# Performance work log

Measured on AMD Instinct MI355X. Metric: run time of the kernel, lower is better.

Reference implementation:

```python
import math
import jax, jax.numpy as jnp
import numpy as np

DILATION = 1  # init_kwargs

def _sep2(x, krow, kcol, d):
    # 2-tap separable correlation with circular 'same' padding:
    # pad-right + conv2d(kernel=[k0,k1]) == k0*x + k1*roll(x, -d, axis)
    xh = kcol[0] * x + kcol[1] * jnp.roll(x, -d, axis=-1)   # along W
    xv = krow[0] * xh + krow[1] * jnp.roll(xh, -d, axis=-2)  # along H
    return xv

def setup_inputs() -> dict:
    key = jax.random.key(0)
    ks = jax.random.split(key, 4)
    B, C, H, W = 8, 64, 256, 256
    LL = jax.random.normal(ks[0], (B, C, H, W), dtype=jnp.float32)
    LH = jax.random.normal(ks[1], (B, C, H, W), dtype=jnp.float32)
    HL = jax.random.normal(ks[2], (B, C, H, W), dtype=jnp.float32)
    HH = jax.random.normal(ks[3], (B, C, H, W), dtype=jnp.float32)
    s = math.sqrt(2.0)
    # torch: lor = [1/s,1/s].flip(0) = [1/s,1/s]; hir = [-1/s,1/s].flip(0) = [1/s,-1/s]
    lor = jnp.array([1.0 / s, 1.0 / s], dtype=jnp.float32)
    hir = jnp.array([1.0 / s, -1.0 / s], dtype=jnp.float32)
    return {"LL": LL, "LH": LH, "HL": HL, "HH": HH, "lor": lor, "hir": hir}

def reference(LL, LH, HL, HH, lor, hir):
    d = DILATION
    rec = (_sep2(LL, lor, lor, d)
           + _sep2(LH, lor, hir, d)
           + _sep2(HL, hir, lor, d)
           + _sep2(HH, hir, hir, d))
    rec = jnp.roll(rec, shift=(1, 1), axis=(-2, -1))
    return 0.25 * rec
```

## Files before the change

kernel.cpp:

```cpp
#include <hip/hip_runtime.h>


static constexpr int HH_ = 256;
static constexpr int WW_ = 256;
static constexpr int RPT = 16;

typedef float f4 __attribute__((ext_vector_type(4)));

__global__ __launch_bounds__(256) void swt_inv_kernel(
    const float* __restrict__ LL, const float* __restrict__ LH,
    const float* __restrict__ HL, const float* __restrict__ HH,
    float* __restrict__ out)
{
    const int slab  = blockIdx.x & 3;
    const int plane = blockIdx.x >> 2;
    const size_t poff = (size_t)plane * (HH_ * WW_);

    const int tx = threadIdx.x & 63;
    const int ty = threadIdx.x >> 6;
    const int w  = tx << 2;
    const int h0 = slab * 64 + ty * RPT;
    const int srcLane = (tx + 63) & 63;

    const float* ll = LL + poff + w;
    const float* lh = LH + poff + w;
    const float* hl = HL + poff + w;
    const float* hh = HH + poff + w;
    float* op = out + poff + w;

    const int hp = (h0 == 0) ? (HH_ - 1) : (h0 - 1);
    f4 Pp, Rp;
    {
        const int r = hp * WW_;
        f4 a = *(const f4*)(ll + r);
        f4 b = *(const f4*)(lh + r);
        f4 c = *(const f4*)(hl + r);
        f4 d = *(const f4*)(hh + r);
        f4 u0 = a + b, u1 = a - b, v0 = c + d, v1 = c - d;
        Pp = u0 + v0;
        Rp = u1 + v1;
    }

    #pragma unroll 4
    for (int i = 0; i < RPT; ++i) {
        const int r = (h0 + i) * WW_;
        f4 a = *(const f4*)(ll + r);
        f4 b = *(const f4*)(lh + r);
        f4 c = *(const f4*)(hl + r);
        f4 d = *(const f4*)(hh + r);

        f4 u0 = a + b, u1 = a - b, v0 = c + d, v1 = c - d;
        f4 Aq = Pp + (u0 - v0);
        f4 Bq = Rp + (u1 - v1);
        Pp = u0 + v0;
        Rp = u1 + v1;

        const float Am = __shfl(Aq.w, srcLane, 64);

        f4 o;
        o.x = 0.125f * (Am   + Bq.x);
        o.y = 0.125f * (Aq.x + Bq.y);
        o.z = 0.125f * (Aq.y + Bq.z);
        o.w = 0.125f * (Aq.z + Bq.w);
        __builtin_nontemporal_store(o, (f4*)(op + r));
    }
}

extern "C" void kernel_launch(void* const* d_in, const int* in_sizes, int n_in,
                              void* d_out, int out_size, void* d_ws, size_t ws_size,
                              hipStream_t stream) {
    const float* LL = (const float*)d_in[0];
    const float* LH = (const float*)d_in[1];
    const float* HL = (const float*)d_in[2];
    const float* HH = (const float*)d_in[3];
    float* out = (float*)d_out;

    const int planes = out_size / (HH_ * WW_);
    dim3 grid(planes * 4);
    dim3 block(256);
    swt_inv_kernel<<<grid, block, 0, stream>>>(LL, LH, HL, HH, out);
}
```

Before: 476.3 us.

## Halve block size, double slabs per plane, and software-prefetch next row

Blocks shrink from 256 to 128 threads, with each plane split into 8 slabs instead of 4, so the grid doubles while each thread still handles 16 rows. The row loop is fully unrolled and now loads row i+1 while computing row i, which hides global load latency behind arithmetic. The cost is more registers for the prefetched values and more redundant halo-row loads across the extra slabs.

```diff
diff --git a/kernel.cpp b/kernel.cpp
--- a/kernel.cpp
+++ b/kernel.cpp
@@ -4,22 +4,23 @@
 static constexpr int HH_ = 256;
 static constexpr int WW_ = 256;
 static constexpr int RPT = 16;
+static constexpr int SLABS = HH_ / (2 * RPT);
 
 typedef float f4 __attribute__((ext_vector_type(4)));
 
-__global__ __launch_bounds__(256) void swt_inv_kernel(
+__global__ __launch_bounds__(128) void swt_inv_kernel(
     const float* __restrict__ LL, const float* __restrict__ LH,
     const float* __restrict__ HL, const float* __restrict__ HH,
     float* __restrict__ out)
 {
-    const int slab  = blockIdx.x & 3;
-    const int plane = blockIdx.x >> 2;
+    const int slab  = blockIdx.x & (SLABS - 1);
+    const int plane = blockIdx.x >> 3;
     const size_t poff = (size_t)plane * (HH_ * WW_);
 
     const int tx = threadIdx.x & 63;
     const int ty = threadIdx.x >> 6;
     const int w  = tx << 2;
-    const int h0 = slab * 64 + ty * RPT;
+    const int h0 = slab * (2 * RPT) + ty * RPT;
     const int srcLane = (tx + 63) & 63;
 
     const float* ll = LL + poff + w;
@@ -41,15 +42,25 @@
         Rp = u1 + v1;
     }
 
-    #pragma unroll 4
+    f4 a0 = *(const f4*)(ll + h0 * WW_);
+    f4 b0 = *(const f4*)(lh + h0 * WW_);
+    f4 c0 = *(const f4*)(hl + h0 * WW_);
+    f4 d0 = *(const f4*)(hh + h0 * WW_);
+
+    #pragma unroll
     for (int i = 0; i < RPT; ++i) {
-        const int r = (h0 + i) * WW_;
-        f4 a = *(const f4*)(ll + r);
-        f4 b = *(const f4*)(lh + r);
-        f4 c = *(const f4*)(hl + r);
-        f4 d = *(const f4*)(hh + r);
+        const int rc = (h0 + i) * WW_;
 
-        f4 u0 = a + b, u1 = a - b, v0 = c + d, v1 = c - d;
+        f4 a1, b1, c1, d1;
+        if (i + 1 < RPT) {
+            const int rn = rc + WW_;
+            a1 = *(const f4*)(ll + rn);
+            b1 = *(const f4*)(lh + rn);
+            c1 = *(const f4*)(hl + rn);
+            d1 = *(const f4*)(hh + rn);
+        }
+
+        f4 u0 = a0 + b0, u1 = a0 - b0, v0 = c0 + d0, v1 = c0 - d0;
         f4 Aq = Pp + (u0 - v0);
         f4 Bq = Rp + (u1 - v1);
         Pp = u0 + v0;
@@ -62,7 +73,9 @@
         o.y = 0.125f * (Aq.x + Bq.y);
         o.z = 0.125f * (Aq.y + Bq.z);
         o.w = 0.125f * (Aq.z + Bq.w);
-        __builtin_nontemporal_store(o, (f4*)(op + r));
+        __builtin_nontemporal_store(o, (f4*)(op + rc));
+
+        a0 = a1; b0 = b1; c0 = c1; d0 = d1;
     }
 }
 
@@ -76,7 +89,7 @@
     float* out = (float*)d_out;
 
     const int planes = out_size / (HH_ * WW_);
-    dim3 grid(planes * 4);
-    dim3 block(256);
+    dim3 grid(planes * SLABS);
+    dim3 block(128);
     swt_inv_kernel<<<grid, block, 0, stream>>>(LL, LH, HL, HH, out);
 }
```

Measured after the change: 474.1 us. No clear change (-0.5%).
